# Optimization experiments

Hardware: AMD Instinct MI355X
Metric: run time of the kernel (lower is better)

## Reference

```python
import jax, jax.numpy as jnp
import numpy as np

N, E, G = 100000, 1600000, 128
IN_DIM, H, C = 329, 4, 64
NEG_SLOPE = 0.2


def setup_inputs() -> dict:
    key = jax.random.key(0)
    ks = jax.random.split(key, 12)
    x = jax.random.normal(ks[0], (N, IN_DIM), dtype=jnp.float32)
    edge_index = jax.random.randint(ks[1], (2, E), 0, N, dtype=jnp.int64)
    batch = jnp.sort(jax.random.randint(ks[2], (N,), 0, G, dtype=jnp.int64))
    s = 1.0 / np.sqrt(IN_DIM)
    W = jax.random.uniform(ks[3], (IN_DIM, H * C), jnp.float32, -s, s)
    att_src = jax.random.normal(ks[4], (H, C), dtype=jnp.float32) * 0.1
    att_dst = jax.random.normal(ks[5], (H, C), dtype=jnp.float32) * 0.1
    bias = jnp.zeros((C,), jnp.float32)
    s1 = 1.0 / np.sqrt(C)
    w1 = jax.random.uniform(ks[6], (C, 64), jnp.float32, -s1, s1)
    b1 = jnp.zeros((64,), jnp.float32)
    s2 = 1.0 / np.sqrt(64)
    w2 = jax.random.uniform(ks[7], (64, 1), jnp.float32, -s2, s2)
    b2 = jnp.zeros((1,), jnp.float32)
    return {"x": x, "W": W, "att_src": att_src, "att_dst": att_dst,
            "bias": bias, "w1": w1, "b1": b1, "w2": w2, "b2": b2,
            "edge_index": edge_index, "batch": batch}


def reference(x, W, att_src, att_dst, bias, w1, b1, w2, b2, edge_index, batch):
    # --- GATConv (heads=4, concat=False, add_self_loops=True) ---
    xp = (x @ W).reshape(N, H, C)                       # [N,H,C]
    a_src = jnp.einsum('nhc,hc->nh', xp, att_src)       # [N,H]
    a_dst = jnp.einsum('nhc,hc->nh', xp, att_dst)       # [N,H]
    loops = jnp.arange(N, dtype=edge_index.dtype)
    src = jnp.concatenate([edge_index[0], loops])       # [E+N]
    dst = jnp.concatenate([edge_index[1], loops])
    logits = jax.nn.leaky_relu(a_src[src] + a_dst[dst], NEG_SLOPE)  # [E+N,H]
    # segment softmax over edges sharing a destination
    mx = jax.ops.segment_max(logits, dst, num_segments=N)
    ex = jnp.exp(logits - mx[dst])
    denom = jax.ops.segment_sum(ex, dst, num_segments=N)
    alpha = ex / denom[dst]                             # [E+N,H]
    msg = xp[src] * alpha[:, :, None]                   # [E+N,H,C]
    agg = jax.ops.segment_sum(msg, dst, num_segments=N) # [N,H,C]
    h = jax.nn.relu(agg.mean(axis=1) + bias)            # [N,C]
    # --- global mean pool over graphs ---
    counts = jax.ops.segment_sum(jnp.ones((N,), h.dtype), batch, num_segments=G)
    g = jax.ops.segment_sum(h, batch, num_segments=G) / jnp.maximum(counts, 1.0)[:, None]
    # --- head MLP ---
    y = jax.nn.sigmoid(jax.nn.relu(g @ w1 + b1) @ w2 + b2)  # [G,1]
    return y
```

## Files before the change

kernel.cpp:

```cpp
#include <hip/hip_runtime.h>
#include <math.h>

#define N_NODES 100000
#define N_EDGES 1600000
#define N_GRAPHS 128
#define IN_DIM 329
#define NH 4
#define CC 64
#define HC 256
#define NEG_SLOPE 0.2f
#define LOG2E 1.44269504f

#define K_PAD 384
#define M_PAD 100096
#define XBYTES (N_NODES * IN_DIM * 4)
#define NBUCK 196
#define BCAP 10240
#define EPB 8192

typedef unsigned short u16;
typedef unsigned char u8;
typedef unsigned int u32;
typedef __attribute__((ext_vector_type(8))) short short8;
typedef __attribute__((ext_vector_type(4))) float floatx4;
typedef __attribute__((ext_vector_type(2))) float floatx2;

__device__ __forceinline__ u16 f2bf(float f) {
    u32 u = __float_as_uint(f);
    u32 r = (u + 0x7FFFu + ((u >> 16) & 1u)) >> 16;
    return (u16)r;
}

__device__ __forceinline__ u32 pkbf(float a, float b) {
    return __builtin_amdgcn_perm(__float_as_uint(b), __float_as_uint(a), 0x07060302u);
}

__device__ __forceinline__ u8 f2fp8(float f) {
#if __has_builtin(__builtin_amdgcn_cvt_pk_fp8_f32)
    int pk = __builtin_amdgcn_cvt_pk_fp8_f32(f, f, 0, false);
    return (u8)(pk & 0xFF);
#else
    u32 u = __float_as_uint(f);
    u32 sgn = (u >> 24) & 0x80;
    float af = fabsf(f);
    if (af >= 448.f) return (u8)(sgn | 0x7E);
    if (af < 0.015625f) {
        int m = (int)rintf(af * 512.f);
        if (m >= 8) return (u8)(sgn | 0x08);
        return (u8)(sgn | (u32)m);
    }
    u32 au = u & 0x7FFFFFFF;
    u32 r = au + 0x0007FFFFu + ((au >> 20) & 1u);
    u32 e = r >> 23;
    u32 m3 = (r >> 20) & 7;
    int fe = (int)e - 127 + 7;
    if (fe >= 16) return (u8)(sgn | 0x7E);
    return (u8)(sgn | ((u32)fe << 3) | m3);
#endif
}

__device__ __forceinline__ float fp82f_sw(u32 b) {
    u32 s = (b & 0x80u) << 24;
    u32 e = (b >> 3) & 0xF;
    u32 m = b & 7;
    if (e == 0) {
        float v = (float)m * 0.001953125f;
        return (b & 0x80) ? -v : v;
    }
    return __uint_as_float(s | ((e + 120) << 23) | (m << 20));
}

__device__ __forceinline__ floatx4 dec4(int p) {
#if __has_builtin(__builtin_amdgcn_cvt_pk_f32_fp8)
    floatx2 lo = __builtin_amdgcn_cvt_pk_f32_fp8(p, false);
    floatx2 hi = __builtin_amdgcn_cvt_pk_f32_fp8(p, true);
    floatx4 r; r.x = lo.x; r.y = lo.y; r.z = hi.x; r.w = hi.y;
    return r;
#else
    floatx4 r;
    r.x = fp82f_sw(p & 0xFF);  r.y = fp82f_sw((p >> 8) & 0xFF);
    r.z = fp82f_sw((p >> 16) & 0xFF); r.w = fp82f_sw((p >> 24) & 0xFF);
    return r;
#endif
}

__device__ __forceinline__ void async_copy16(const void* g, void* l) {
    __builtin_amdgcn_global_load_lds((const __attribute__((address_space(1))) void*)g,
                                     (__attribute__((address_space(3))) void*)l, 16, 0, 0);
}

__global__ __launch_bounds__(256) void convw_kernel(const float* __restrict__ W, u16* __restrict__ WbT)
{
    int i = blockIdx.x * 256 + threadIdx.x;
    if (i >= HC * 96) return;
    int c = i / 96;
    int k0 = (i - c * 96) * 4;
    ushort4 o = {0, 0, 0, 0};
    const float* wp = W + c;
    if (k0 < IN_DIM)     o.x = f2bf(wp[(size_t)k0 * HC]);
    if (k0 + 1 < IN_DIM) o.y = f2bf(wp[(size_t)(k0 + 1) * HC]);
    if (k0 + 2 < IN_DIM) o.z = f2bf(wp[(size_t)(k0 + 2) * HC]);
    if (k0 + 3 < IN_DIM) o.w = f2bf(wp[(size_t)(k0 + 3) * HC]);
    *(ushort4*)(WbT + (size_t)c * K_PAD + k0) = o;
}

__global__ __launch_bounds__(256) void gemm_mfma_kernel(
    const float* __restrict__ x, const u16* __restrict__ WbT, u8* __restrict__ xp8)
{
    __shared__ float Asf[128 * 64];
    __shared__ u16 Bs[128 * 64];

    const int tid = threadIdx.x;
    const int lane = tid & 63;
    const int wave = tid >> 6;
    const int lr = lane & 15;
    const int q = lane >> 4;
    const int row0 = blockIdx.x * 128;
    const int col0 = blockIdx.y * 128;
    const int rm0 = (wave & 1) * 64;
    const int cn0 = (wave >> 1) * 64;

    floatx4 acc[4][4];
#pragma unroll
    for (int i = 0; i < 4; i++)
#pragma unroll
        for (int j = 0; j < 4; j++) {
            acc[i][j].x = 0.f; acc[i][j].y = 0.f; acc[i][j].z = 0.f; acc[i][j].w = 0.f;
        }

    for (int k0 = 0; k0 < K_PAD; k0 += 64) {
#pragma unroll
        for (int t = 0; t < 8; t++) {
            int chunk = tid + t * 256;
            int row = chunk >> 4, ch = chunk & 15;
            int chl = ch ^ (row & 15);
            long gb = (long)(row0 + row) * (IN_DIM * 4) + (long)k0 * 4 + chl * 16;
            if (gb > (long)XBYTES - 16) gb = (long)XBYTES - 16;
            async_copy16((const char*)x + gb, (char*)Asf + (size_t)chunk * 16);
        }
#pragma unroll
        for (int t = 0; t < 4; t++) {
            int off = (tid + t * 256) * 16;
            int row = off >> 7;
            int col = off & 127;
            int gcol = col ^ ((row & 7) * 16);
            const char* gb = (const char*)WbT + (size_t)(col0 + row) * (K_PAD * 2) + k0 * 2 + gcol;
            async_copy16(gb, (char*)Bs + off);
        }
        __syncthreads();

        short8 af[2][4], bf[2][4];
#pragma unroll
        for (int ks = 0; ks < 2; ks++) {
#pragma unroll
            for (int i = 0; i < 4; i++) {
                int ra = rm0 + i * 16 + lr;
                int c0 = ks * 8 + q * 2;
                int sw = ra & 15;
                const float4* base = (const float4*)(Asf + ra * 64);
                float4 lo = base[c0 ^ sw];
                float4 hi = base[(c0 ^ sw) ^ 1];
                union { short8 v; u32 w[4]; } fr;
                fr.w[0] = pkbf(lo.x, lo.y);
                fr.w[1] = pkbf(lo.z, lo.w);
                fr.w[2] = pkbf(hi.x, hi.y);
                fr.w[3] = pkbf(hi.z, hi.w);
                af[ks][i] = fr.v;

                int rb = cn0 + i * 16 + lr;
                int cb = (ks * 64 + q * 16) ^ ((rb & 7) * 16);
                bf[ks][i] = *(const short8*)((const char*)Bs + rb * 128 + cb);
            }
        }
#pragma unroll
        for (int ks = 0; ks < 2; ks++)
#pragma unroll
            for (int i = 0; i < 4; i++)
#pragma unroll
                for (int j = 0; j < 4; j++)
                    acc[i][j] = __builtin_amdgcn_mfma_f32_16x16x32_bf16(af[ks][i], bf[ks][j], acc[i][j], 0, 0, 0);
        __syncthreads();
    }

#pragma unroll
    for (int i = 0; i < 4; i++) {
#pragma unroll
        for (int j = 0; j < 4; j++) {
            int col = col0 + cn0 + j * 16 + lr;
            float v[4] = {acc[i][j].x, acc[i][j].y, acc[i][j].z, acc[i][j].w};
#pragma unroll
            for (int r = 0; r < 4; r++) {
                int row = row0 + rm0 + i * 16 + q * 4 + r;
                if (row < N_NODES) xp8[(size_t)row * HC + col] = f2fp8(v[r]);
            }
        }
    }
}

__global__ __launch_bounds__(256) void a8_kernel(
    const u8* __restrict__ xp8, const float* __restrict__ att_src, const float* __restrict__ att_dst,
    float* __restrict__ a_src, float* __restrict__ a_dst)
{
    int n = blockIdx.x * 4 + (threadIdx.x >> 6);
    int lane = threadIdx.x & 63;
    if (n >= N_NODES) return;
    int h = lane >> 4;
    int c0 = (lane & 15) * 4;
    int p = *(const int*)(xp8 + (size_t)n * HC + h * CC + c0);
    floatx4 v = dec4(p);
    const float* as = att_src + h * CC + c0;
    const float* ad = att_dst + h * CC + c0;
    float ps = v.x * as[0] + v.y * as[1] + v.z * as[2] + v.w * as[3];
    float pd = v.x * ad[0] + v.y * ad[1] + v.z * ad[2] + v.w * ad[3];
#pragma unroll
    for (int m = 1; m < 16; m <<= 1) {
        ps += __shfl_xor(ps, m, 64);
        pd += __shfl_xor(pd, m, 64);
    }
    if ((lane & 15) == 0) {
        a_src[n * 4 + h] = ps * LOG2E;
        a_dst[n * 4 + h] = pd * LOG2E;
    }
}

__global__ __launch_bounds__(256) void bin2_kernel(
    const int* __restrict__ ei, int* __restrict__ bcur, int2* __restrict__ bins)
{
    __shared__ int hist[NBUCK];
    __shared__ int gpos[NBUCK];
    __shared__ int lcur[NBUCK];
    __shared__ int sc[256];

    const int t = threadIdx.x;
    const int lo = blockIdx.x * EPB;
    const int hi = min(lo + EPB, N_EDGES + N_NODES);

    for (int b = t; b < NBUCK; b += 256) hist[b] = 0;
    __syncthreads();

    for (int i = lo + t; i < hi; i += 256) {
        int d = (i < N_EDGES) ? ei[N_EDGES + i] : (i - N_EDGES);
        atomicAdd(&hist[d >> 9], 1);
    }
    __syncthreads();

    int v = (t < NBUCK) ? hist[t] : 0;
    if (t < NBUCK) { gpos[t] = atomicAdd(&bcur[t], v); lcur[t] = 0; }
    (void)sc;
    __syncthreads();

    for (int i = lo + t; i < hi; i += 256) {
        int s, d;
        if (i < N_EDGES) { s = ei[i]; d = ei[N_EDGES + i]; }
        else             { s = i - N_EDGES; d = s; }
        int b = d >> 9;
        int pos = gpos[b] + atomicAdd(&lcur[b], 1);
        if (pos < BCAP) {
            int2 r; r.x = s; r.y = d;
            bins[(size_t)b * BCAP + pos] = r;
        }
    }
}

__global__ __launch_bounds__(512) void fill3_kernel(
    const int* __restrict__ bcur, const int2* __restrict__ bins,
    int2* __restrict__ rs_deg, int* __restrict__ csr)
{
    __shared__ int deg[512];
    __shared__ int cur[512];
    __shared__ int sc[256];
    __shared__ int order[BCAP];

    const int t = threadIdx.x;
    const int b = blockIdx.x;
    const int cnt = min(bcur[b], BCAP);
    const int2* bp = bins + (size_t)b * BCAP;
    const int gbase = b * BCAP;

    deg[t] = 0;
    __syncthreads();
    for (int i = t; i < cnt; i += 512) atomicAdd(&deg[bp[i].y & 511], 1);
    __syncthreads();

    int d0 = 0, d1 = 0;
    if (t < 256) {
        d0 = deg[2 * t]; d1 = deg[2 * t + 1];
        sc[t] = d0 + d1;
    }
    __syncthreads();
    for (int off = 1; off < 256; off <<= 1) {
        int u = (t < 256 && t >= off) ? sc[t - off] : 0;
        __syncthreads();
        if (t < 256) sc[t] += u;
        __syncthreads();
    }
    if (t < 256) {
        int excl = sc[t] - (d0 + d1);
        cur[2 * t] = excl;
        cur[2 * t + 1] = excl + d0;
        int n0 = b * 512 + 2 * t;
        if (n0 < N_NODES)     { int2 rd; rd.x = gbase + excl;      rd.y = d0; rs_deg[n0] = rd; }
        if (n0 + 1 < N_NODES) { int2 rd; rd.x = gbase + excl + d0; rd.y = d1; rs_deg[n0 + 1] = rd; }
    }
    __syncthreads();

    for (int i = t; i < cnt; i += 512) {
        int2 r = bp[i];
        int pos = atomicAdd(&cur[r.y & 511], 1);
        order[pos] = r.x;
    }
    __syncthreads();

    for (int i = t; i < cnt; i += 512) csr[gbase + i] = order[i];
}

__global__ __launch_bounds__(256) void aggregate_kernel(
    const u8* __restrict__ xp8, const float* __restrict__ a_src, const float* __restrict__ a_dst,
    const int2* __restrict__ rs_deg, const int* __restrict__ csr,
    const float* __restrict__ bias, float* __restrict__ hbuf)
{
    int n = blockIdx.x * 4 + (threadIdx.x >> 6);
    int lane = threadIdx.x & 63;
    if (n >= N_NODES) return;
    int2 rd = rs_deg[n];
    int rstart = __builtin_amdgcn_readfirstlane(rd.x);
    int deg    = __builtin_amdgcn_readfirstlane(rd.y);
    const int* ep = csr + rstart;
    int h = lane >> 4;
    int xoff = lane * 4;

    float ad = a_dst[n * 4 + h];

    const int dm1 = deg - 1;
    const int nb  = (deg + 3) >> 2;

    float acc0 = 0.f, acc1 = 0.f, acc2 = 0.f, acc3 = 0.f, den = 0.f;

    int iA0, iA1, iA2, iA3;
    int iB0 = 0, iB1 = 0, iB2 = 0, iB3 = 0;
    float aa0, aa1, aa2, aa3;  int pa0, pa1, pa2, pa3;
    float ab0, ab1, ab2, ab3;  int pb0, pb1, pb2, pb3;

#define AGG_LDI(eb_, j0, j1, j2, j3) do { \
        j0 = ep[min((eb_), dm1)];     j1 = ep[min((eb_) + 1, dm1)]; \
        j2 = ep[min((eb_) + 2, dm1)]; j3 = ep[min((eb_) + 3, dm1)]; } while (0)

#define AGG_LDD(j0, j1, j2, j3, a0_, a1_, a2_, a3_, q0_, q1_, q2_, q3_) do { \
        a0_ = a_src[(size_t)(j0) * 4 + h];  q0_ = *(const int*)(xp8 + (size_t)(j0) * HC + xoff); \
        a1_ = a_src[(size_t)(j1) * 4 + h];  q1_ = *(const int*)(xp8 + (size_t)(j1) * HC + xoff); \
        a2_ = a_src[(size_t)(j2) * 4 + h];  q2_ = *(const int*)(xp8 + (size_t)(j2) * HC + xoff); \
        a3_ = a_src[(size_t)(j3) * 4 + h];  q3_ = *(const int*)(xp8 + (size_t)(j3) * HC + xoff); } while (0)

#define AGG_CMP(eb_, a0_, a1_, a2_, a3_, q0_, q1_, q2_, q3_) do { \
        float z0 = a0_ + ad, z1 = a1_ + ad, z2 = a2_ + ad, z3 = a3_ + ad; \
        float w0 = exp2f(fmaxf(z0, NEG_SLOPE * z0)); \
        float w1 = exp2f(fmaxf(z1, NEG_SLOPE * z1)); \
        float w2 = exp2f(fmaxf(z2, NEG_SLOPE * z2)); \
        float w3 = exp2f(fmaxf(z3, NEG_SLOPE * z3)); \
        if ((eb_) + 3 >= deg) {                \
            if ((eb_) + 1 >= deg) w1 = 0.f; \
            if ((eb_) + 2 >= deg) w2 = 0.f; \
            if ((eb_) + 3 >= deg) w3 = 0.f; \
        } \
        den += (w0 + w1) + (w2 + w3); \
        floatx4 v0 = dec4(q0_), v1 = dec4(q1_), v2 = dec4(q2_), v3 = dec4(q3_); \
        acc0 = fmaf(w0, v0.x, acc0); acc1 = fmaf(w0, v0.y, acc1); \
        acc2 = fmaf(w0, v0.z, acc2); acc3 = fmaf(w0, v0.w, acc3); \
        acc0 = fmaf(w1, v1.x, acc0); acc1 = fmaf(w1, v1.y, acc1); \
        acc2 = fmaf(w1, v1.z, acc2); acc3 = fmaf(w1, v1.w, acc3); \
        acc0 = fmaf(w2, v2.x, acc0); acc1 = fmaf(w2, v2.y, acc1); \
        acc2 = fmaf(w2, v2.z, acc2); acc3 = fmaf(w2, v2.w, acc3); \
        acc0 = fmaf(w3, v3.x, acc0); acc1 = fmaf(w3, v3.y, acc1); \
        acc2 = fmaf(w3, v3.z, acc2); acc3 = fmaf(w3, v3.w, acc3); } while (0)

    AGG_LDI(0, iA0, iA1, iA2, iA3);
    AGG_LDD(iA0, iA1, iA2, iA3, aa0, aa1, aa2, aa3, pa0, pa1, pa2, pa3);
    if (nb > 1) AGG_LDI(4, iB0, iB1, iB2, iB3);

    for (int b = 0; b < nb; b += 2) {
        int eb = b * 4;
        if (b + 1 < nb) AGG_LDD(iB0, iB1, iB2, iB3, ab0, ab1, ab2, ab3, pb0, pb1, pb2, pb3);
        if (b + 2 < nb) AGG_LDI(eb + 8, iA0, iA1, iA2, iA3);
        AGG_CMP(eb, aa0, aa1, aa2, aa3, pa0, pa1, pa2, pa3);
        if (b + 1 < nb) {
            if (b + 2 < nb) AGG_LDD(iA0, iA1, iA2, iA3, aa0, aa1, aa2, aa3, pa0, pa1, pa2, pa3);
            if (b + 3 < nb) AGG_LDI(eb + 12, iB0, iB1, iB2, iB3);
            AGG_CMP(eb + 4, ab0, ab1, ab2, ab3, pb0, pb1, pb2, pb3);
        }
    }

#undef AGG_LDI
#undef AGG_LDD
#undef AGG_CMP

    float r = 1.f / den;
    acc0 *= r; acc1 *= r; acc2 *= r; acc3 *= r;
#pragma unroll
    for (int m = 16; m <= 32; m <<= 1) {
        acc0 += __shfl_xor(acc0, m, 64);
        acc1 += __shfl_xor(acc1, m, 64);
        acc2 += __shfl_xor(acc2, m, 64);
        acc3 += __shfl_xor(acc3, m, 64);
    }
    if (lane < 16) {
        const float* bp = bias + lane * 4;
        float4 o;
        o.x = fmaxf(0.25f * acc0 + bp[0], 0.f);
        o.y = fmaxf(0.25f * acc1 + bp[1], 0.f);
        o.z = fmaxf(0.25f * acc2 + bp[2], 0.f);
        o.w = fmaxf(0.25f * acc3 + bp[3], 0.f);
        *(float4*)&hbuf[(size_t)n * CC + lane * 4] = o;
    }
}

__global__ __launch_bounds__(256) void pool1_kernel(
    const float* __restrict__ hbuf, const int* __restrict__ batch,
    float* __restrict__ gsum, int* __restrict__ gcnt)
{
    int w = threadIdx.x >> 6, lane = threadIdx.x & 63;
    int r0 = blockIdx.x * 128 + w * 32;
    if (r0 >= N_NODES) return;
    int r1 = min(r0 + 32, N_NODES);
    int cur = batch[r0];
    float s = 0.f;
    int c = 0;
    for (int r = r0; r < r1; r++) {
        int bb = batch[r];
        if (bb != cur) {
            atomicAdd(&gsum[cur * 64 + lane], s);
            if (lane == 0) atomicAdd(&gcnt[cur], c);
            s = 0.f; c = 0; cur = bb;
        }
        s += hbuf[(size_t)r * CC + lane];
        c++;
    }
    atomicAdd(&gsum[cur * 64 + lane], s);
    if (lane == 0) atomicAdd(&gcnt[cur], c);
}

__global__ __launch_bounds__(64) void pool2_kernel(
    const float* __restrict__ gsum, const int* __restrict__ gcnt,
    const float* __restrict__ w1, const float* __restrict__ b1,
    const float* __restrict__ w2, const float* __restrict__ b2,
    float* __restrict__ out)
{
    int g = blockIdx.x;
    int lane = threadIdx.x;
    __shared__ float gv[64];
    gv[lane] = gsum[g * 64 + lane] / (float)max(gcnt[g], 1);
    __syncthreads();
    float hid = b1[lane];
    for (int c = 0; c < 64; c++) hid = fmaf(gv[c], w1[c * 64 + lane], hid);
    hid = fmaxf(hid, 0.f);
    float part = hid * w2[lane];
#pragma unroll
    for (int off = 32; off > 0; off >>= 1) part += __shfl_xor(part, off, 64);
    if (lane == 0) out[g] = 1.f / (1.f + __expf(-(part + b2[0])));
}

extern "C" void kernel_launch(void* const* d_in, const int* in_sizes, int n_in,
                              void* d_out, int out_size, void* d_ws, size_t ws_size,
                              hipStream_t stream)
{
    const float* x       = (const float*)d_in[0];
    const float* W       = (const float*)d_in[1];
    const float* att_src = (const float*)d_in[2];
    const float* att_dst = (const float*)d_in[3];
    const float* bias    = (const float*)d_in[4];
    const float* w1      = (const float*)d_in[5];
    const float* b1      = (const float*)d_in[6];
    const float* w2      = (const float*)d_in[7];
    const float* b2      = (const float*)d_in[8];
    const int*   ei      = (const int*)d_in[9];
    const int*   batch   = (const int*)d_in[10];
    float* out = (float*)d_out;

    char* ws = (char*)d_ws;
    size_t off = 0;
    auto alloc = [&](size_t bytes) -> void* {
        void* p = ws + off;
        off += (bytes + 255) & ~(size_t)255;
        return p;
    };
    u16*   WbT       = (u16*)alloc((size_t)HC * K_PAD * 2);
    u8*    xp8       = (u8*)alloc((size_t)N_NODES * HC);
    float* a_src_b   = (float*)alloc((size_t)N_NODES * NH * 4);
    float* a_dst_b   = (float*)alloc((size_t)N_NODES * NH * 4);
    size_t zoff0 = off;
    int*   bcur      = (int*)alloc((size_t)NBUCK * 4);
    float* gsum      = (float*)alloc((size_t)N_GRAPHS * 64 * 4);
    int*   gcnt      = (int*)alloc((size_t)N_GRAPHS * 4);
    size_t zbytes = off - zoff0;
    int2*  bins      = (int2*)alloc((size_t)NBUCK * BCAP * 8);
    int2*  rs_deg    = (int2*)alloc((size_t)N_NODES * 8);
    int*   csr       = (int*)alloc((size_t)NBUCK * BCAP * 4);
    float* hbuf      = (float*)alloc((size_t)N_NODES * CC * 4);

    hipMemsetAsync(bcur, 0, zbytes, stream);

    convw_kernel<<<(HC * 96 + 255) / 256, 256, 0, stream>>>(W, WbT);

    dim3 ggrid(M_PAD / 128, 2);
    gemm_mfma_kernel<<<ggrid, 256, 0, stream>>>(x, WbT, xp8);

    a8_kernel<<<(N_NODES + 3) / 4, 256, 0, stream>>>(xp8, att_src, att_dst, a_src_b, a_dst_b);

    int tot = N_EDGES + N_NODES;
    bin2_kernel<<<(tot + EPB - 1) / EPB, 256, 0, stream>>>(ei, bcur, bins);
    fill3_kernel<<<NBUCK, 512, 0, stream>>>(bcur, bins, rs_deg, csr);

    aggregate_kernel<<<(N_NODES + 3) / 4, 256, 0, stream>>>(xp8, a_src_b, a_dst_b,
                                                            rs_deg, csr, bias, hbuf);

    pool1_kernel<<<(N_NODES + 127) / 128, 256, 0, stream>>>(hbuf, batch, gsum, gcnt);
    pool2_kernel<<<N_GRAPHS, 64, 0, stream>>>(gsum, gcnt, w1, b1, w2, b2, out);
}
```

Before: 409.9 us.

## Double-buffer GEMM tiles with register-staged A and bf16 conversion at store

The GEMM kernel now double-buffers both A and B shared tiles. A is loaded into registers for the next k-step while MFMAs run on the current one, then converted to bf16 once and stored to shared memory. This replaces the fp32 A tile that every wave re-converted on each fragment read. The aim is to overlap global loads with compute and shrink shared-memory footprint and traffic for A, at the cost of extra registers (8 float4) and possibly lower occupancy.

```diff
diff --git a/kernel.cpp b/kernel.cpp
--- a/kernel.cpp
+++ b/kernel.cpp
@@ -107,8 +107,8 @@
 __global__ __launch_bounds__(256) void gemm_mfma_kernel(
     const float* __restrict__ x, const u16* __restrict__ WbT, u8* __restrict__ xp8)
 {
-    __shared__ float Asf[128 * 64];
-    __shared__ u16 Bs[128 * 64];
+    __shared__ u16 Ab[2][128 * 64];
+    __shared__ u16 Bb[2][128 * 64];
 
     const int tid = threadIdx.x;
     const int lane = tid & 63;
@@ -120,6 +120,9 @@
     const int rm0 = (wave & 1) * 64;
     const int cn0 = (wave >> 1) * 64;
 
+    const int arow = tid >> 1;
+    const int ahalf = tid & 1;
+
     floatx4 acc[4][4];
 #pragma unroll
     for (int i = 0; i < 4; i++)
@@ -128,26 +131,55 @@
             acc[i][j].x = 0.f; acc[i][j].y = 0.f; acc[i][j].z = 0.f; acc[i][j].w = 0.f;
         }
 
-    for (int k0 = 0; k0 < K_PAD; k0 += 64) {
-#pragma unroll
-        for (int t = 0; t < 8; t++) {
-            int chunk = tid + t * 256;
-            int row = chunk >> 4, ch = chunk & 15;
-            int chl = ch ^ (row & 15);
-            long gb = (long)(row0 + row) * (IN_DIM * 4) + (long)k0 * 4 + chl * 16;
+    float4 ar[8];
+
+    auto aload = [&](int k0) {
+#pragma unroll
+        for (int i = 0; i < 8; i++) {
+            long gb = (long)(row0 + arow) * (IN_DIM * 4) + (long)k0 * 4 + ahalf * 128 + i * 16;
             if (gb > (long)XBYTES - 16) gb = (long)XBYTES - 16;
-            async_copy16((const char*)x + gb, (char*)Asf + (size_t)chunk * 16);
-        }
+            ar[i] = *(const float4*)((const char*)x + gb);
+        }
+    };
+    auto apack = [&](int buf) {
+        char* base = (char*)(&Ab[buf][0]) + arow * 128;
+#pragma unroll
+        for (int j = 0; j < 4; j++) {
+            float4 lo = ar[2 * j], hi = ar[2 * j + 1];
+            union { uint4 v; u32 w[4]; } st;
+            st.w[0] = pkbf(lo.x, lo.y);
+            st.w[1] = pkbf(lo.z, lo.w);
+            st.w[2] = pkbf(hi.x, hi.y);
+            st.w[3] = pkbf(hi.z, hi.w);
+            int c = (ahalf * 4 + j) ^ (arow & 7);
+            *(uint4*)(base + c * 16) = st.v;
+        }
+    };
+    auto bstage = [&](int k0, int buf) {
 #pragma unroll
         for (int t = 0; t < 4; t++) {
             int off = (tid + t * 256) * 16;
-            int row = off >> 7;
-            int col = off & 127;
-            int gcol = col ^ ((row & 7) * 16);
-            const char* gb = (const char*)WbT + (size_t)(col0 + row) * (K_PAD * 2) + k0 * 2 + gcol;
-            async_copy16(gb, (char*)Bs + off);
-        }
-        __syncthreads();
+            int rowb = off >> 7;
+            int colb = off & 127;
+            int gcol = colb ^ ((rowb & 7) * 16);
+            const char* gb = (const char*)WbT + (size_t)(col0 + rowb) * (K_PAD * 2) + k0 * 2 + gcol;
+            async_copy16(gb, (char*)(&Bb[buf][0]) + off);
+        }
+    };
+
+    aload(0);
+    bstage(0, 0);
+    apack(0);
+    asm volatile("s_waitcnt vmcnt(0)" ::: "memory");
+    __syncthreads();
+
+    int cur = 0;
+    for (int k0 = 0; k0 < K_PAD; k0 += 64) {
+        const bool more = (k0 + 64 < K_PAD);
+        if (more) { aload(k0 + 64); bstage(k0 + 64, cur ^ 1); }
+
+        const char* Abase = (const char*)(&Ab[cur][0]);
+        const char* Bbase = (const char*)(&Bb[cur][0]);
 
         short8 af[2][4], bf[2][4];
 #pragma unroll
@@ -155,21 +187,9 @@
 #pragma unroll
             for (int i = 0; i < 4; i++) {
                 int ra = rm0 + i * 16 + lr;
-                int c0 = ks * 8 + q * 2;
-                int sw = ra & 15;
-                const float4* base = (const float4*)(Asf + ra * 64);
-                float4 lo = base[c0 ^ sw];
-                float4 hi = base[(c0 ^ sw) ^ 1];
-                union { short8 v; u32 w[4]; } fr;
-                fr.w[0] = pkbf(lo.x, lo.y);
-                fr.w[1] = pkbf(lo.z, lo.w);
-                fr.w[2] = pkbf(hi.x, hi.y);
-                fr.w[3] = pkbf(hi.z, hi.w);
-                af[ks][i] = fr.v;
-
+                af[ks][i] = *(const short8*)(Abase + ra * 128 + (((ks * 4 + q) ^ (ra & 7)) * 16));
                 int rb = cn0 + i * 16 + lr;
-                int cb = (ks * 64 + q * 16) ^ ((rb & 7) * 16);
-                bf[ks][i] = *(const short8*)((const char*)Bs + rb * 128 + cb);
+                bf[ks][i] = *(const short8*)(Bbase + rb * 128 + ((ks * 64 + q * 16) ^ ((rb & 7) * 16)));
             }
         }
 #pragma unroll
@@ -179,7 +199,11 @@
 #pragma unroll
                 for (int j = 0; j < 4; j++)
                     acc[i][j] = __builtin_amdgcn_mfma_f32_16x16x32_bf16(af[ks][i], bf[ks][j], acc[i][j], 0, 0, 0);
+
+        if (more) apack(cur ^ 1);
+        asm volatile("s_waitcnt vmcnt(0)" ::: "memory");
         __syncthreads();
+        cur ^= 1;
     }
 
 #pragma unroll
```

Measured after the change: 460.1 us. 1.12x slower.
